# Kernel optimization log

Hardware: AMD Instinct MI355X
Metric: run time of the kernel (lower is better)

Reference implementation:

```python
import jax, jax.numpy as jnp
import numpy as np

# Dims (match init_kwargs / input_specs)
N, N_REP, K, D = 8, 2048, 16, 3
C_IN, C_LIFT = 64, 64
C_MID = C_IN + C_LIFT   # 128
C_OUT = 128             # groups=C_OUT -> depthwise since C_MID == C_OUT
EPS = 1e-5


def setup_inputs() -> dict:
    key = jax.random.key(0)
    ks = jax.random.split(key, 10)
    w = lambda i, shape, fan_in: (jax.random.uniform(ks[i], shape, dtype=jnp.float32) * 2.0 - 1.0) / np.float32(np.sqrt(fan_in))
    return dict(
        p=jax.random.normal(ks[0], (N, N_REP, D), dtype=jnp.float32),
        P=jax.random.normal(ks[1], (N, N_REP, K, D), dtype=jnp.float32),
        F=jax.random.normal(ks[2], (N, N_REP, K, C_IN), dtype=jnp.float32),
        # BatchNorm over the D spatial channels (training-mode stats)
        bn_gamma=jnp.ones((D,), dtype=jnp.float32),
        bn_beta=jnp.zeros((D,), dtype=jnp.float32),
        # mlp_lift: Dense(D->C_LIFT) + Dense(C_LIFT->C_LIFT), ELU each
        lift_w1=w(3, (D, C_LIFT), D), lift_b1=jnp.zeros((C_LIFT,), dtype=jnp.float32),
        lift_w2=w(4, (C_LIFT, C_LIFT), C_LIFT), lift_b2=jnp.zeros((C_LIFT,), dtype=jnp.float32),
        # mid_conv: 1x1 Conv2d(D -> K) channels-last == Linear on last dim
        mid_w=w(5, (D, K), D), mid_b=jnp.zeros((K,), dtype=jnp.float32),
        # mlp: Dense(K->K) with ELU
        mlp_w=w(6, (K, K), K), mlp_b=jnp.zeros((K,), dtype=jnp.float32),
        # end_conv: Conv2d(C_MID -> C_OUT, kernel (K,1), groups=C_OUT) == depthwise
        # reduction over the neighbor dim; weight per (out_channel, neighbor)
        end_w=w(7, (C_OUT, K), K), end_b=jnp.zeros((C_OUT,), dtype=jnp.float32),
    )


def reference(p, P, F, bn_gamma, bn_beta, lift_w1, lift_b1, lift_w2, lift_b2,
              mid_w, mid_b, mlp_w, mlp_b, end_w, end_b):
    # Center neighborhoods on the representative point
    P_local = P - p[:, :, None, :]                              # (N,R,K,D)
    # Channels-last BatchNorm over D, batch stats over (N,R,K)
    mean = jnp.mean(P_local, axis=(0, 1, 2), keepdims=True)
    var = jnp.var(P_local, axis=(0, 1, 2), keepdims=True)
    P_norm = (P_local - mean) * jax.lax.rsqrt(var + EPS) * bn_gamma + bn_beta
    # Lift spatial coords to C_LIFT features (MLP of Dense+ELU layers)
    F_lift = jax.nn.elu(P_norm @ lift_w1 + lift_b1)
    F_lift = jax.nn.elu(F_lift @ lift_w2 + lift_b2)             # (N,R,K,C_LIFT)
    F_cat = jnp.concatenate([F_lift, F], axis=-1)               # (N,R,K,C_MID)
    # X-transform: 1x1 conv D->K then Dense(K->K)+ELU -> (N,R,K,K)
    X = P_norm @ mid_w + mid_b
    X = jax.nn.elu(X @ mlp_w + mlp_b)
    # Weighted aggregation: small batched matmul over the neighbor dim
    F_X = jnp.einsum('nrkj,nrjc->nrkc', X, F_cat)               # (N,R,K,C_MID)
    # Depthwise end conv: per-channel weighted sum over neighbors
    F_p = jnp.einsum('nrkc,ck->nrc', F_X, end_w) + end_b        # (N,R,C_OUT)
    return F_p
```

## Files before the change

kernel.cpp:

```cpp
#include <hip/hip_runtime.h>
#include <cstddef>

#define N_TOT   8
#define R_TOT   2048
#define KK      16
#define CL      64
#define CM      128
#define EPSV    1e-5f
#define CNTF    262144.0f

typedef float    f32x4  __attribute__((ext_vector_type(4)));
typedef short    bf16x8 __attribute__((ext_vector_type(8)));
typedef unsigned u32x4  __attribute__((ext_vector_type(4)));

union FragU { bf16x8 f; unsigned u[4]; };

__device__ float    g_w1f[72*4];
__device__ unsigned g_w2p[8*64*4];
__device__ float    g_bn[8];

__device__ __forceinline__ float elu_f(float x){
    return x > 0.f ? x : (__expf(x) - 1.f);
}

#if defined(__has_builtin) && __has_builtin(__builtin_amdgcn_cvt_pk_bf16_f32)
__device__ __forceinline__ unsigned pk_bf16(float a, float b){
    auto v = __builtin_amdgcn_cvt_pk_bf16_f32(a, b);
    unsigned u; __builtin_memcpy(&u, &v, 4);
    return u;
}
#else
__device__ __forceinline__ unsigned pk_bf16(float a, float b){
    unsigned ua = __float_as_uint(a), ub = __float_as_uint(b);
    ua += 0x7fff + ((ua >> 16) & 1);
    ub += 0x7fff + ((ub >> 16) & 1);
    return (ua >> 16) | (ub & 0xffff0000u);
}
#endif
__device__ __forceinline__ float bf_lo(unsigned u){ return __uint_as_float(u << 16); }
__device__ __forceinline__ float bf_hi(unsigned u){ return __uint_as_float(u & 0xffff0000u); }

__device__ __forceinline__ void split4(const float* x, unsigned* o){
    unsigned h01 = pk_bf16(x[0], x[1]);
    unsigned h23 = pk_bf16(x[2], x[3]);
    float l0 = x[0] - bf_lo(h01), l1 = x[1] - bf_hi(h01);
    float l2 = x[2] - bf_lo(h23), l3 = x[3] - bf_hi(h23);
    o[0] = h01; o[1] = h23; o[2] = pk_bf16(l0, l1); o[3] = pk_bf16(l2, l3);
}

__global__ __launch_bounds__(256) void xconv_stats(
    const float* __restrict__ p, const float* __restrict__ P,
    const float* __restrict__ w1, const float* __restrict__ b1,
    const float* __restrict__ w2, float* __restrict__ ws)
{
    const int tid = threadIdx.x;
    const int g = blockIdx.x*256 + tid;
    const float4* P4 = (const float4*)(P + (size_t)g*12);
    float4 a = P4[0], b = P4[1], c = P4[2];
    const int nr = g >> 2;
    float pp0 = p[nr*3], pp1 = p[nr*3+1], pp2 = p[nr*3+2];
    float vx0=a.x-pp0, vx1=a.w-pp0, vx2=b.z-pp0, vx3=c.y-pp0;
    float vy0=a.y-pp1, vy1=b.x-pp1, vy2=b.w-pp1, vy3=c.z-pp1;
    float vz0=a.z-pp2, vz1=b.y-pp2, vz2=c.x-pp2, vz3=c.w-pp2;
    float s1[3], s2[3];
    s1[0]=vx0+vx1+vx2+vx3; s2[0]=vx0*vx0+vx1*vx1+vx2*vx2+vx3*vx3;
    s1[1]=vy0+vy1+vy2+vy3; s2[1]=vy0*vy0+vy1*vy1+vy2*vy2+vy3*vy3;
    s1[2]=vz0+vz1+vz2+vz3; s2[2]=vz0*vz0+vz1*vz1+vz2*vz2+vz3*vz3;

    #pragma unroll
    for (int off = 32; off > 0; off >>= 1){
        #pragma unroll
        for (int d = 0; d < 3; d++){
            s1[d] += __shfl_down(s1[d], off, 64);
            s2[d] += __shfl_down(s2[d], off, 64);
        }
    }
    __shared__ float red[4][6];
    int wave = tid >> 6, lane = tid & 63;
    if (lane == 0){
        #pragma unroll
        for (int d = 0; d < 3; d++){ red[wave][d] = s1[d]; red[wave][3+d] = s2[d]; }
    }
    __syncthreads();
    float v = 0.f;
    if (tid < 6) v = red[0][tid] + red[1][tid] + red[2][tid] + red[3][tid];
    if (tid < 8) ws[blockIdx.x*8 + tid] = v;

    if (blockIdx.x == 0){
        if (wave == 0){
            f32x4 w4 = { w1[lane], w1[64+lane], w1[128+lane], b1[lane] };
            *(f32x4*)&g_w1f[((lane>>3)*9 + (lane&7))*4] = w4;
        } else if (wave == 1){
            const int lo16 = lane & 15, quad = lane >> 4;
            #pragma unroll
            for (int bb = 0; bb < 4; bb++)
                #pragma unroll
                for (int s = 0; s < 2; s++){
                    u32x4 f;
                    #pragma unroll
                    for (int d = 0; d < 4; d++){
                        int q0 = s*32 + quad*8 + d*2;
                        int idx = q0*64 + bb*16 + lo16;
                        f[d] = pk_bf16(w2[idx], w2[idx + 64]);
                    }
                    *(u32x4*)&g_w2p[((bb*2 + s)*64 + lane)*4] = f;
                }
        }
    }
}

__global__ __launch_bounds__(64) void xconv_bn(
    const float* __restrict__ ws,
    const float* __restrict__ gamma, const float* __restrict__ beta)
{
    const int lane = threadIdx.x;
    float s1[3] = {0.f,0.f,0.f}, s2[3] = {0.f,0.f,0.f};
    const f32x4* wp = (const f32x4*)ws;
    #pragma unroll
    for (int i = 0; i < 4; i++){
        int row = lane + i*64;
        f32x4 pa = wp[row*2], pb = wp[row*2 + 1];
        s1[0] += pa.x; s1[1] += pa.y; s1[2] += pa.z;
        s2[0] += pa.w; s2[1] += pb.x; s2[2] += pb.y;
    }
    #pragma unroll
    for (int off = 32; off > 0; off >>= 1){
        #pragma unroll
        for (int d = 0; d < 3; d++){
            s1[d] += __shfl_xor(s1[d], off, 64);
            s2[d] += __shfl_xor(s2[d], off, 64);
        }
    }
    if (lane == 0){
        #pragma unroll
        for (int d = 0; d < 3; d++){
            float mean = s1[d] * (1.0f/CNTF);
            float var  = s2[d] * (1.0f/CNTF) - mean*mean;
            float s    = gamma[d] * rsqrtf(var + EPSV);
            g_bn[d] = s; g_bn[3+d] = beta[d] - mean*s;
        }
        g_bn[6] = 0.f; g_bn[7] = 0.f;
    }
}

__global__ __launch_bounds__(256, 5) void xconv_main(
    const float* __restrict__ p,   const float* __restrict__ P,
    const float* __restrict__ F,
    const float* __restrict__ mlpw,const float* __restrict__ mlpb,
    const float* __restrict__ midw,const float* __restrict__ midb,
    const float* __restrict__ b2,
    const float* __restrict__ endw,const float* __restrict__ endb,
    float* __restrict__ out)
{
    __shared__ float    sEndw[128*20];
    __shared__ float    sW1f[72*4];
    __shared__ unsigned sW2[8*64*4];
    __shared__ float    sMid[16*4];

    const int tid  = threadIdx.x;
    const int lane = tid & 63;
    const int lo16 = lane & 15;
    const int quad = lane >> 4;
    const int wave = tid >> 6;

    if (wave == 0){
        *(f32x4*)&sW1f[lane*4] = *(const f32x4*)&g_w1f[lane*4];
        if (lane < 8)
            *(f32x4*)&sW1f[(64+lane)*4] = *(const f32x4*)&g_w1f[(64+lane)*4];
    } else if (wave == 1){
        #pragma unroll
        for (int i = 0; i < 8; i++)
            *(u32x4*)&sW2[(i*64+lane)*4] = *(const u32x4*)&g_w2p[(i*64+lane)*4];
    } else {
        int c = tid - 128;
        const f32x4* ep = (const f32x4*)endw;
        #pragma unroll
        for (int i = 0; i < 4; i++)
            *(f32x4*)&sEndw[c*20 + i*4] = ep[c*4 + i];
        if (c >= 112){
            int m2 = c - 112;
            f32x4 mv = { midw[m2], midw[16+m2], midw[32+m2], midb[m2] };
            *(f32x4*)&sMid[m2*4] = mv;
        }
    }

    f32x4 bn0 = *(const f32x4*)&g_bn[0];
    float sc0 = bn0.x, sc1 = bn0.y, sc2 = bn0.z, sh0 = bn0.w;
    float sh1 = g_bn[4], sh2 = g_bn[5];

    FragU mlpA[2];
    {
        float mw[4];
        #pragma unroll
        for (int r = 0; r < 4; r++) mw[r] = mlpw[(quad*4 + r)*16 + lo16];
        unsigned o[4]; split4(mw, o);
        mlpA[0].u[0]=o[0]; mlpA[0].u[1]=o[1]; mlpA[0].u[2]=o[0]; mlpA[0].u[3]=o[1];
        mlpA[1].u[0]=o[2]; mlpA[1].u[1]=o[3]; mlpA[1].u[2]=o[2]; mlpA[1].u[3]=o[3];
    }
    float mlpbr[4];
    #pragma unroll
    for (int r = 0; r < 4; r++) mlpbr[r] = mlpb[quad*4 + r];
    float b2r[4];
    #pragma unroll
    for (int b = 0; b < 4; b++) b2r[b] = b2[b*16 + lo16];
    const float endb0 = endb[lane], endb1 = endb[64 + lane];

    __syncthreads();

    const int nr = blockIdx.x*4 + wave;

    const int pb = nr*48 + lo16*3;
    float P0 = P[pb], P1 = P[pb+1], P2 = P[pb+2];
    float pp0 = p[nr*3], pp1 = p[nr*3+1], pp2 = p[nr*3+2];

    unsigned fh01[4], fh23[4];
    #pragma unroll
    for (int bt = 0; bt < 4; bt++){
        const size_t fb = (size_t)nr*1024 + (size_t)(quad*4)*64 + bt*16 + lo16;
        float f0 = F[fb], f1 = F[fb + 64], f2 = F[fb + 128], f3 = F[fb + 192];
        fh01[bt] = pk_bf16(f0, f1);
        fh23[bt] = pk_bf16(f2, f3);
    }

    const float pn0 = (P0 - pp0)*sc0 + sh0;
    const float pn1 = (P1 - pp1)*sc1 + sh1;
    const float pn2 = (P2 - pp2)*sc2 + sh2;

    FragU hf[2];
    #pragma unroll
    for (int s = 0; s < 2; s++){
        const f32x4* wp = (const f32x4*)&sW1f[((s*4 + quad)*9)*4];
        #pragma unroll
        for (int d = 0; d < 4; d++){
            f32x4 wa = wp[2*d], wb = wp[2*d+1];
            float h0  = fmaf(pn2, wa.z, fmaf(pn1, wa.y, fmaf(pn0, wa.x, wa.w)));
            float h1v = fmaf(pn2, wb.z, fmaf(pn1, wb.y, fmaf(pn0, wb.x, wb.w)));
            hf[s].u[d] = pk_bf16(elu_f(h0), elu_f(h1v));
        }
    }

    float x0[4];
    #pragma unroll
    for (int j = 0; j < 4; j++){
        f32x4 mw = *(const f32x4*)&sMid[(quad*4 + j)*4];
        x0[j] = fmaf(pn2, mw.z, fmaf(pn1, mw.y, fmaf(pn0, mw.x, mw.w)));
    }
    FragU x0f; split4(x0, x0f.u);

    f32x4 dx = {0.f,0.f,0.f,0.f};
    dx = __builtin_amdgcn_mfma_f32_16x16x32_bf16(mlpA[0].f, x0f.f, dx, 0,0,0);
    dx = __builtin_amdgcn_mfma_f32_16x16x32_bf16(mlpA[1].f, x0f.f, dx, 0,0,0);
    float xv[4];
    #pragma unroll
    for (int r = 0; r < 4; r++) xv[r] = elu_f(dx[r] + mlpbr[r]);
    FragU xA; split4(xv, xA.u);

    float o0 = 0.f, o1 = 0.f;

    #pragma unroll
    for (int b = 0; b < 4; b++){
        FragU wf0, wf1;
        *(u32x4*)wf0.u = *(const u32x4*)&sW2[((b*2 + 0)*64 + lane)*4];
        *(u32x4*)wf1.u = *(const u32x4*)&sW2[((b*2 + 1)*64 + lane)*4];
        f32x4 dl = {0.f,0.f,0.f,0.f};
        dl = __builtin_amdgcn_mfma_f32_16x16x32_bf16(hf[0].f, wf0.f, dl, 0,0,0);
        dl = __builtin_amdgcn_mfma_f32_16x16x32_bf16(hf[1].f, wf1.f, dl, 0,0,0);
        float fl[4];
        #pragma unroll
        for (int r = 0; r < 4; r++) fl[r] = elu_f(dl[r] + b2r[b]);
        FragU bfg;
        unsigned h01 = pk_bf16(fl[0], fl[1]), h23 = pk_bf16(fl[2], fl[3]);
        bfg.u[0] = h01; bfg.u[1] = h23; bfg.u[2] = h01; bfg.u[3] = h23;
        f32x4 da = {0.f,0.f,0.f,0.f};
        da = __builtin_amdgcn_mfma_f32_16x16x32_bf16(xA.f, bfg.f, da, 0,0,0);
        const float4 ew = *(const float4*)&sEndw[(b*16 + lo16)*20 + quad*4];
        float pt = da[0]*ew.x + da[1]*ew.y + da[2]*ew.z + da[3]*ew.w;
        pt += __shfl_xor(pt, 16, 64);
        pt += __shfl_xor(pt, 32, 64);
        if (b == quad) o0 = pt;
    }
    #pragma unroll
    for (int bt = 0; bt < 4; bt++){
        FragU bfg;
        bfg.u[0] = fh01[bt]; bfg.u[1] = fh23[bt];
        bfg.u[2] = fh01[bt]; bfg.u[3] = fh23[bt];
        f32x4 da = {0.f,0.f,0.f,0.f};
        da = __builtin_amdgcn_mfma_f32_16x16x32_bf16(xA.f, bfg.f, da, 0,0,0);
        const float4 ew = *(const float4*)&sEndw[(64 + bt*16 + lo16)*20 + quad*4];
        float pt = da[0]*ew.x + da[1]*ew.y + da[2]*ew.z + da[3]*ew.w;
        pt += __shfl_xor(pt, 16, 64);
        pt += __shfl_xor(pt, 32, 64);
        if (bt == quad) o1 = pt;
    }

    out[(size_t)nr*CM + lane]      = o0 + endb0;
    out[(size_t)nr*CM + 64 + lane] = o1 + endb1;
}

extern "C" void kernel_launch(void* const* d_in, const int* in_sizes, int n_in,
                              void* d_out, int out_size, void* d_ws, size_t ws_size,
                              hipStream_t stream)
{
    const float* p     = (const float*)d_in[0];
    const float* P     = (const float*)d_in[1];
    const float* F     = (const float*)d_in[2];
    const float* gamma = (const float*)d_in[3];
    const float* beta  = (const float*)d_in[4];
    const float* w1    = (const float*)d_in[5];
    const float* b1    = (const float*)d_in[6];
    const float* w2    = (const float*)d_in[7];
    const float* b2    = (const float*)d_in[8];
    const float* midw  = (const float*)d_in[9];
    const float* midb  = (const float*)d_in[10];
    const float* mlpw  = (const float*)d_in[11];
    const float* mlpb  = (const float*)d_in[12];
    const float* endw  = (const float*)d_in[13];
    const float* endb  = (const float*)d_in[14];
    float* ws  = (float*)d_ws;
    float* out = (float*)d_out;

    xconv_stats<<<256, 256, 0, stream>>>(p, P, w1, b1, w2, ws);
    xconv_bn   <<<1,    64, 0, stream>>>(ws, gamma, beta);
    xconv_main <<<4096, 256, 0, stream>>>(p, P, F, mlpw, mlpb, midw, midb,
                                          b2, endw, endb, out);
}
```

Measured before the change: 139.5 us.

## Fuse BN finalize into stats kernel via last-block atomic; vectorize F loads

Removes the separate single-block BN finalize launch: each stats block bumps a global counter, and the last block to arrive reduces the partials and writes the scale and shift. F is now read as float4 loads per lane rather than scalar strided loads. The end-weight rows in shared memory are permuted and lane outputs gathered with a shuffle so results still land on the right channels. This removes one kernel launch and widens global loads, but relies on threadfence/atomic ordering and a correctly reset counter.

Measured after the change: 142.6 us. 1.02x slower.

```diff
diff --git a/kernel.cpp b/kernel.cpp
--- a/kernel.cpp
+++ b/kernel.cpp
@@ -18,6 +18,7 @@
 __device__ float    g_w1f[72*4];
 __device__ unsigned g_w2p[8*64*4];
 __device__ float    g_bn[8];
+__device__ unsigned g_cnt = 0;
 
 __device__ __forceinline__ float elu_f(float x){
     return x > 0.f ? x : (__expf(x) - 1.f);
@@ -51,7 +52,9 @@
 __global__ __launch_bounds__(256) void xconv_stats(
     const float* __restrict__ p, const float* __restrict__ P,
     const float* __restrict__ w1, const float* __restrict__ b1,
-    const float* __restrict__ w2, float* __restrict__ ws)
+    const float* __restrict__ w2,
+    const float* __restrict__ gamma, const float* __restrict__ beta,
+    float* __restrict__ ws)
 {
     const int tid = threadIdx.x;
     const int g = blockIdx.x*256 + tid;
@@ -76,15 +79,19 @@
         }
     }
     __shared__ float red[4][6];
+    __shared__ int   sLast;
     int wave = tid >> 6, lane = tid & 63;
     if (lane == 0){
         #pragma unroll
         for (int d = 0; d < 3; d++){ red[wave][d] = s1[d]; red[wave][3+d] = s2[d]; }
     }
     __syncthreads();
-    float v = 0.f;
-    if (tid < 6) v = red[0][tid] + red[1][tid] + red[2][tid] + red[3][tid];
-    if (tid < 8) ws[blockIdx.x*8 + tid] = v;
+    if (tid < 8){
+        float v = 0.f;
+        if (tid < 6) v = red[0][tid] + red[1][tid] + red[2][tid] + red[3][tid];
+        ws[blockIdx.x*8 + tid] = v;
+        __threadfence();
+    }
 
     if (blockIdx.x == 0){
         if (wave == 0){
@@ -107,39 +114,43 @@
                 }
         }
     }
-}
-
-__global__ __launch_bounds__(64) void xconv_bn(
-    const float* __restrict__ ws,
-    const float* __restrict__ gamma, const float* __restrict__ beta)
-{
-    const int lane = threadIdx.x;
-    float s1[3] = {0.f,0.f,0.f}, s2[3] = {0.f,0.f,0.f};
-    const f32x4* wp = (const f32x4*)ws;
-    #pragma unroll
-    for (int i = 0; i < 4; i++){
-        int row = lane + i*64;
-        f32x4 pa = wp[row*2], pb = wp[row*2 + 1];
-        s1[0] += pa.x; s1[1] += pa.y; s1[2] += pa.z;
-        s2[0] += pa.w; s2[1] += pb.x; s2[2] += pb.y;
-    }
-    #pragma unroll
-    for (int off = 32; off > 0; off >>= 1){
-        #pragma unroll
-        for (int d = 0; d < 3; d++){
-            s1[d] += __shfl_xor(s1[d], off, 64);
-            s2[d] += __shfl_xor(s2[d], off, 64);
-        }
-    }
-    if (lane == 0){
-        #pragma unroll
-        for (int d = 0; d < 3; d++){
-            float mean = s1[d] * (1.0f/CNTF);
-            float var  = s2[d] * (1.0f/CNTF) - mean*mean;
-            float s    = gamma[d] * rsqrtf(var + EPSV);
-            g_bn[d] = s; g_bn[3+d] = beta[d] - mean*s;
-        }
-        g_bn[6] = 0.f; g_bn[7] = 0.f;
+
+    __syncthreads();
+    if (tid == 0){
+        unsigned old = atomicAdd(&g_cnt, 1u);
+        sLast = (old == 255u);
+        if (sLast) atomicExch(&g_cnt, 0u);
+    }
+    __syncthreads();
+    if (sLast && tid < 64){
+        __threadfence();
+        float t1[3] = {0.f,0.f,0.f}, t2[3] = {0.f,0.f,0.f};
+        const f32x4* wp = (const f32x4*)ws;
+        #pragma unroll
+        for (int i = 0; i < 4; i++){
+            int row = tid + i*64;
+            f32x4 pa = wp[row*2], pb = wp[row*2 + 1];
+            t1[0] += pa.x; t1[1] += pa.y; t1[2] += pa.z;
+            t2[0] += pa.w; t2[1] += pb.x; t2[2] += pb.y;
+        }
+        #pragma unroll
+        for (int off = 32; off > 0; off >>= 1){
+            #pragma unroll
+            for (int d = 0; d < 3; d++){
+                t1[d] += __shfl_xor(t1[d], off, 64);
+                t2[d] += __shfl_xor(t2[d], off, 64);
+            }
+        }
+        if (tid == 0){
+            #pragma unroll
+            for (int d = 0; d < 3; d++){
+                float mean = t1[d] * (1.0f/CNTF);
+                float var  = t2[d] * (1.0f/CNTF) - mean*mean;
+                float s    = gamma[d] * rsqrtf(var + EPSV);
+                g_bn[d] = s; g_bn[3+d] = beta[d] - mean*s;
+            }
+            g_bn[6] = 0.f; g_bn[7] = 0.f;
+        }
     }
 }
 
@@ -173,10 +184,11 @@
             *(u32x4*)&sW2[(i*64+lane)*4] = *(const u32x4*)&g_w2p[(i*64+lane)*4];
     } else {
         int c = tid - 128;
+        int row = (c < 64) ? c : 64 + ((c-64)&3)*16 + ((c-64)>>2);
         const f32x4* ep = (const f32x4*)endw;
         #pragma unroll
         for (int i = 0; i < 4; i++)
-            *(f32x4*)&sEndw[c*20 + i*4] = ep[c*4 + i];
+            *(f32x4*)&sEndw[row*20 + i*4] = ep[c*4 + i];
         if (c >= 112){
             int m2 = c - 112;
             f32x4 mv = { midw[m2], midw[16+m2], midw[32+m2], midb[m2] };
@@ -213,14 +225,12 @@
     float P0 = P[pb], P1 = P[pb+1], P2 = P[pb+2];
     float pp0 = p[nr*3], pp1 = p[nr*3+1], pp2 = p[nr*3+2];
 
-    unsigned fh01[4], fh23[4];
-    #pragma unroll
-    for (int bt = 0; bt < 4; bt++){
-        const size_t fb = (size_t)nr*1024 + (size_t)(quad*4)*64 + bt*16 + lo16;
-        float f0 = F[fb], f1 = F[fb + 64], f2 = F[fb + 128], f3 = F[fb + 192];
-        fh01[bt] = pk_bf16(f0, f1);
-        fh23[bt] = pk_bf16(f2, f3);
-    }
+    const float4* fp = (const float4*)(F + (size_t)nr*1024 + (size_t)(quad*4)*64);
+    float4 q0 = fp[lo16], q1 = fp[16+lo16], q2 = fp[32+lo16], q3 = fp[48+lo16];
+    unsigned fh01[4] = { pk_bf16(q0.x,q1.x), pk_bf16(q0.y,q1.y),
+                         pk_bf16(q0.z,q1.z), pk_bf16(q0.w,q1.w) };
+    unsigned fh23[4] = { pk_bf16(q2.x,q3.x), pk_bf16(q2.y,q3.y),
+                         pk_bf16(q2.z,q3.z), pk_bf16(q2.w,q3.w) };
 
     const float pn0 = (P0 - pp0)*sc0 + sh0;
     const float pn1 = (P1 - pp1)*sc1 + sh1;
@@ -255,7 +265,7 @@
     for (int r = 0; r < 4; r++) xv[r] = elu_f(dx[r] + mlpbr[r]);
     FragU xA; split4(xv, xA.u);
 
-    float o0 = 0.f, o1 = 0.f;
+    float o0 = 0.f;
 
     #pragma unroll
     for (int b = 0; b < 4; b++){
@@ -279,19 +289,26 @@
         pt += __shfl_xor(pt, 32, 64);
         if (b == quad) o0 = pt;
     }
-    #pragma unroll
-    for (int bt = 0; bt < 4; bt++){
+    float pt4[4];
+    #pragma unroll
+    for (int g = 0; g < 4; g++){
         FragU bfg;
-        bfg.u[0] = fh01[bt]; bfg.u[1] = fh23[bt];
-        bfg.u[2] = fh01[bt]; bfg.u[3] = fh23[bt];
+        bfg.u[0] = fh01[g]; bfg.u[1] = fh23[g];
+        bfg.u[2] = fh01[g]; bfg.u[3] = fh23[g];
         f32x4 da = {0.f,0.f,0.f,0.f};
         da = __builtin_amdgcn_mfma_f32_16x16x32_bf16(xA.f, bfg.f, da, 0,0,0);
-        const float4 ew = *(const float4*)&sEndw[(64 + bt*16 + lo16)*20 + quad*4];
+        const float4 ew = *(const float4*)&sEndw[(64 + g*16 + lo16)*20 + quad*4];
         float pt = da[0]*ew.x + da[1]*ew.y + da[2]*ew.z + da[3]*ew.w;
         pt += __shfl_xor(pt, 16, 64);
         pt += __shfl_xor(pt, 32, 64);
-        if (bt == quad) o1 = pt;
-    }
+        pt4[g] = pt;
+    }
+    const int src = quad*20 + (lo16 >> 2);
+    float t0 = __shfl(pt4[0], src, 64), t1 = __shfl(pt4[1], src, 64);
+    float t2 = __shfl(pt4[2], src, 64), t3 = __shfl(pt4[3], src, 64);
+    float ta = (lo16 & 1) ? t1 : t0;
+    float tb = (lo16 & 1) ? t3 : t2;
+    float o1 = (lo16 & 2) ? tb : ta;
 
     out[(size_t)nr*CM + lane]      = o0 + endb0;
     out[(size_t)nr*CM + 64 + lane] = o1 + endb1;
@@ -319,8 +336,7 @@
     float* ws  = (float*)d_ws;
     float* out = (float*)d_out;
 
-    xconv_stats<<<256, 256, 0, stream>>>(p, P, w1, b1, w2, ws);
-    xconv_bn   <<<1,    64, 0, stream>>>(ws, gamma, beta);
+    xconv_stats<<<256, 256, 0, stream>>>(p, P, w1, b1, w2, gamma, beta, ws);
     xconv_main <<<4096, 256, 0, stream>>>(p, P, F, mlpw, mlpb, midw, midb,
                                           b2, endw, endb, out);
 }
```
